# Optimization experiments

Hardware: AMD Instinct MI355X
Metric: run time of the kernel (lower is better)

## Reference

```python
import jax, jax.numpy as jnp
import numpy as np

EPS = 1e-5

def setup_inputs() -> dict:
    key = jax.random.key(0)
    ks = jax.random.split(key, 12)
    B, S = 48, 1024
    x = jax.random.normal(ks[0], (3, B, S, 3), dtype=jnp.float32)
    # stacked per-band projection weights: index 0=a, 1=b, 2=c
    WQ = jax.random.normal(ks[1], (3, 3, 3), dtype=jnp.float32) * 0.3
    bQ = jax.random.normal(ks[2], (3, 3), dtype=jnp.float32) * 0.1
    WK = jax.random.normal(ks[3], (3, 3, 3), dtype=jnp.float32) * 0.3
    bK = jax.random.normal(ks[4], (3, 3), dtype=jnp.float32) * 0.1
    WV = jax.random.normal(ks[5], (3, 3, 3), dtype=jnp.float32) * 0.3
    bV = jax.random.normal(ks[6], (3, 3), dtype=jnp.float32) * 0.1
    bn_gamma = jnp.ones((9,), dtype=jnp.float32)
    bn_beta = jnp.zeros((9,), dtype=jnp.float32)
    fc_w = jax.random.normal(ks[7], (3, 9), dtype=jnp.float32) * 0.3
    fc_b = jax.random.normal(ks[8], (3,), dtype=jnp.float32) * 0.1
    return dict(x=x, WQ=WQ, bQ=bQ, WK=WK, bK=bK, WV=WV, bV=bV,
                bn_gamma=bn_gamma, bn_beta=bn_beta, fc_w=fc_w, fc_b=fc_b)

def _attn(Q, K, V):
    # Q,K,V: (B, S, 3)
    scores = jnp.einsum('bsd,btd->bst', Q, K) / jnp.sqrt(jnp.float32(3.0))
    w = jax.nn.softmax(scores, axis=-1)
    return jnp.einsum('bst,btd->bsd', w, V)

def reference(x, WQ, bQ, WK, bK, WV, bV, bn_gamma, bn_beta, fc_w, fc_b):
    # x: (3, B, S, 3) -> per-band xs[n]: (B, S, 3)
    xs = x  # band axis already leading
    # per-band projections: Q[n] = xs[n] @ WQ[n].T + bQ[n]
    Q = jnp.einsum('nbsd,ned->nbse', xs, WQ) + bQ[:, None, None, :]
    K = jnp.einsum('nbsd,ned->nbse', xs, WK) + bK[:, None, None, :]
    V = jnp.einsum('nbsd,ned->nbse', xs, WV) + bV[:, None, None, :]
    a1 = _attn(Q[2], K[0], V[1])  # Q_c, K_a, V_b
    a2 = _attn(Q[0], K[1], V[2])  # Q_a, K_b, V_c
    a3 = _attn(Q[1], K[2], V[0])  # Q_b, K_c, V_a
    out = jnp.concatenate([a1, a2, a3], axis=-1)  # (B, S, 9)
    flat = out.reshape(-1, 9)
    # BatchNorm1d (training-mode batch statistics, biased variance)
    mean = jnp.mean(flat, axis=0)
    var = jnp.var(flat, axis=0)
    normed = (flat - mean) / jnp.sqrt(var + EPS) * bn_gamma + bn_beta
    y = normed @ fc_w.T + fc_b  # (B*S, 3)
    return y.reshape(-1, 3, 3)
```

## Files before the change

kernel.cpp:

```cpp
#include <hip/hip_runtime.h>
#include <math.h>

#define BB 48
#define SS 1024
#define NCB (3 * BB)
#define NROW (BB * SS)
#define NBLK2 (NROW / 256)

typedef float f32x2 __attribute__((ext_vector_type(2)));


template <int KSv>
__global__ __launch_bounds__(256) void mbfca_attn(
    const float* __restrict__ x,
    const float* __restrict__ WQ, const float* __restrict__ bQ,
    const float* __restrict__ WK, const float* __restrict__ bK,
    const float* __restrict__ WV, const float* __restrict__ bV,
    float* __restrict__ part)
{
    constexpr int SSK = SS / KSv;
    const int bid   = blockIdx.x;
    const int slice = bid % KSv;
    const int cb    = bid / KSv;
    const int c     = cb / BB;
    const int b     = cb % BB;
    const int kband = c;
    const int vband = (c + 1) % 3;
    const int qband = (c + 2) % 3;

    __shared__ __align__(16) float Ksm[3][SSK];
    __shared__ __align__(16) float Vsm[3][SSK];

    const int tid = threadIdx.x;

    float wk[9], wv[9], wq[9], bk[3], bv[3], bq[3];
    #pragma unroll
    for (int i = 0; i < 9; ++i) {
        wk[i] = WK[kband * 9 + i];
        wv[i] = WV[vband * 9 + i];
        wq[i] = WQ[qband * 9 + i];
    }
    #pragma unroll
    for (int i = 0; i < 3; ++i) {
        bk[i] = bK[kband * 3 + i];
        bv[i] = bV[vband * 3 + i];
        bq[i] = bQ[qband * 3 + i];
    }

    const float* xk = x + (size_t)(kband * BB + b) * SS * 3;
    const float* xv = x + (size_t)(vband * BB + b) * SS * 3;
    const float* xq = x + (size_t)(qband * BB + b) * SS * 3;

    for (int t = tid; t < SSK; t += 256) {
        const int tk = slice * SSK + t;
        float a0 = xk[tk * 3 + 0], a1 = xk[tk * 3 + 1], a2 = xk[tk * 3 + 2];
        Ksm[0][t] = wk[0] * a0 + wk[1] * a1 + wk[2] * a2 + bk[0];
        Ksm[1][t] = wk[3] * a0 + wk[4] * a1 + wk[5] * a2 + bk[1];
        Ksm[2][t] = wk[6] * a0 + wk[7] * a1 + wk[8] * a2 + bk[2];
        float c0 = xv[tk * 3 + 0], c1 = xv[tk * 3 + 1], c2 = xv[tk * 3 + 2];
        Vsm[0][t] = wv[0] * c0 + wv[1] * c1 + wv[2] * c2 + bv[0];
        Vsm[1][t] = wv[3] * c0 + wv[4] * c1 + wv[5] * c2 + bv[1];
        Vsm[2][t] = wv[6] * c0 + wv[7] * c1 + wv[8] * c2 + bv[2];
    }
    __syncthreads();

    const float qscale = 0.57735026918962576f * 1.4426950408889634f;
    f32x2 qp0[4], qp1[4], qp2[4];
    {
        const float4* xq4 = reinterpret_cast<const float4*>(xq + 12 * tid);
        float4 A = xq4[0], B4 = xq4[1], C4 = xq4[2];
        float a[12] = {A.x, A.y, A.z, A.w, B4.x, B4.y, B4.z, B4.w,
                       C4.x, C4.y, C4.z, C4.w};
        #pragma unroll
        for (int j = 0; j < 4; ++j) {
            float a0 = a[j * 3 + 0], a1 = a[j * 3 + 1], a2 = a[j * 3 + 2];
            float t0 = (wq[0] * a0 + wq[1] * a1 + wq[2] * a2 + bq[0]) * qscale;
            float t1 = (wq[3] * a0 + wq[4] * a1 + wq[5] * a2 + bq[1]) * qscale;
            float t2 = (wq[6] * a0 + wq[7] * a1 + wq[8] * a2 + bq[2]) * qscale;
            qp0[j] = (f32x2){t0, t0};
            qp1[j] = (f32x2){t1, t1};
            qp2[j] = (f32x2){t2, t2};
        }
    }

    f32x2 lac[4], a0[4], a1[4], a2[4];
    #pragma unroll
    for (int j = 0; j < 4; ++j) {
        lac[j] = (f32x2){0.f, 0.f};
        a0[j]  = (f32x2){0.f, 0.f};
        a1[j]  = (f32x2){0.f, 0.f};
        a2[j]  = (f32x2){0.f, 0.f};
    }

    const float4* K0 = reinterpret_cast<const float4*>(&Ksm[0][0]);
    const float4* K1 = reinterpret_cast<const float4*>(&Ksm[1][0]);
    const float4* K2 = reinterpret_cast<const float4*>(&Ksm[2][0]);
    const float4* V0 = reinterpret_cast<const float4*>(&Vsm[0][0]);
    const float4* V1 = reinterpret_cast<const float4*>(&Vsm[1][0]);
    const float4* V2 = reinterpret_cast<const float4*>(&Vsm[2][0]);

    for (int t4 = 0; t4 < SSK / 4; ++t4) {
        float4 k0 = K0[t4], k1 = K1[t4], k2 = K2[t4];
        float4 v0 = V0[t4], v1 = V1[t4], v2 = V2[t4];
        f32x2 k0l = {k0.x, k0.y}, k0h = {k0.z, k0.w};
        f32x2 k1l = {k1.x, k1.y}, k1h = {k1.z, k1.w};
        f32x2 k2l = {k2.x, k2.y}, k2h = {k2.z, k2.w};
        f32x2 v0l = {v0.x, v0.y}, v0h = {v0.z, v0.w};
        f32x2 v1l = {v1.x, v1.y}, v1h = {v1.z, v1.w};
        f32x2 v2l = {v2.x, v2.y}, v2h = {v2.z, v2.w};
        #pragma unroll
        for (int j = 0; j < 4; ++j) {
            f32x2 sl = qp0[j] * k0l + qp1[j] * k1l + qp2[j] * k2l;
            f32x2 sh = qp0[j] * k0h + qp1[j] * k1h + qp2[j] * k2h;
            f32x2 pl, ph;
            pl.x = __builtin_amdgcn_exp2f(sl.x);
            pl.y = __builtin_amdgcn_exp2f(sl.y);
            ph.x = __builtin_amdgcn_exp2f(sh.x);
            ph.y = __builtin_amdgcn_exp2f(sh.y);
            lac[j] += pl + ph;
            a0[j]  += pl * v0l + ph * v0h;
            a1[j]  += pl * v1l + ph * v1h;
            a2[j]  += pl * v2l + ph * v2h;
        }
    }

    float4* dst = reinterpret_cast<float4*>(part) +
                  ((size_t)(slice * NCB + cb) * SS + 4 * tid);
    #pragma unroll
    for (int j = 0; j < 4; ++j)
        dst[j] = make_float4(a0[j].x + a0[j].y,
                             a1[j].x + a1[j].y,
                             a2[j].x + a2[j].y,
                             lac[j].x + lac[j].y);
}

template <int KSv>
__global__ __launch_bounds__(256) void mbfca_stats(
    float* __restrict__ part, float* __restrict__ partial)
{
    const int r = blockIdx.x * 256 + threadIdx.x;
    const int b = r >> 10, s = r & 1023;
    __shared__ float red[4][18];

    float sums[18];
    #pragma unroll
    for (int k = 0; k < 18; ++k) sums[k] = 0.f;

    float4* p4 = reinterpret_cast<float4*>(part);
    #pragma unroll
    for (int c = 0; c < 3; ++c) {
        const int cb = c * BB + b;
        float4 t = make_float4(0.f, 0.f, 0.f, 0.f);
        #pragma unroll
        for (int sl = 0; sl < KSv; ++sl) {
            float4 u = p4[(size_t)(sl * NCB + cb) * SS + s];
            t.x += u.x; t.y += u.y; t.z += u.z; t.w += u.w;
        }
        float inv = 1.0f / t.w;
        float o0 = t.x * inv, o1 = t.y * inv, o2 = t.z * inv;
        p4[(size_t)cb * SS + s] = make_float4(o0, o1, o2, 0.f);
        sums[3 * c + 0] = o0;          sums[3 * c + 1] = o1;          sums[3 * c + 2] = o2;
        sums[9 + 3 * c + 0] = o0 * o0; sums[9 + 3 * c + 1] = o1 * o1; sums[9 + 3 * c + 2] = o2 * o2;
    }

    #pragma unroll
    for (int off = 32; off >= 1; off >>= 1)
        #pragma unroll
        for (int k = 0; k < 18; ++k)
            sums[k] += __shfl_xor(sums[k], off, 64);

    const int tid = threadIdx.x;
    if ((tid & 63) == 0) {
        #pragma unroll
        for (int k = 0; k < 18; ++k) red[tid >> 6][k] = sums[k];
    }
    __syncthreads();
    if (tid < 18)
        partial[blockIdx.x * 18 + tid] =
            red[0][tid] + red[1][tid] + red[2][tid] + red[3][tid];
}

__global__ __launch_bounds__(256) void mbfca_bnfc(
    const float* __restrict__ part, const float* __restrict__ partial,
    const float* __restrict__ gamma, const float* __restrict__ beta,
    const float* __restrict__ fcw, const float* __restrict__ fcb,
    float* __restrict__ out)
{
    __shared__ float red[4][18];
    __shared__ float accs[18];
    const int tid = threadIdx.x;

    float sums[18];
    #pragma unroll
    for (int k = 0; k < 18; ++k) sums[k] = 0.f;
    if (tid < NBLK2) {
        #pragma unroll
        for (int k = 0; k < 18; ++k) sums[k] = partial[tid * 18 + k];
    }
    #pragma unroll
    for (int off = 32; off >= 1; off >>= 1)
        #pragma unroll
        for (int k = 0; k < 18; ++k)
            sums[k] += __shfl_xor(sums[k], off, 64);
    if ((tid & 63) == 0) {
        #pragma unroll
        for (int k = 0; k < 18; ++k) red[tid >> 6][k] = sums[k];
    }
    __syncthreads();
    if (tid < 18)
        accs[tid] = red[0][tid] + red[1][tid] + red[2][tid] + red[3][tid];
    __syncthreads();

    const int r = blockIdx.x * 256 + tid;
    const int b = r >> 10, s = r & 1023;
    const float invN = 1.0f / (float)NROW;

    float sc[9], sh[9];
    #pragma unroll
    for (int ch = 0; ch < 9; ++ch) {
        float mean = accs[ch] * invN;
        float var  = accs[9 + ch] * invN - mean * mean;
        float sfac = gamma[ch] * rsqrtf(var + 1e-5f);
        sc[ch] = sfac;
        sh[ch] = beta[ch] - mean * sfac;
    }

    const float4* p4 = reinterpret_cast<const float4*>(part);
    float y0 = fcb[0], y1 = fcb[1], y2 = fcb[2];
    #pragma unroll
    for (int c = 0; c < 3; ++c) {
        const int cb = c * BB + b;
        float4 t = p4[(size_t)cb * SS + s];
        float o[3] = {t.x, t.y, t.z};
        #pragma unroll
        for (int e = 0; e < 3; ++e) {
            float n = o[e] * sc[3 * c + e] + sh[3 * c + e];
            y0 += n * fcw[3 * c + e];
            y1 += n * fcw[9 + 3 * c + e];
            y2 += n * fcw[18 + 3 * c + e];
        }
    }
    out[r * 3 + 0] = y0;
    out[r * 3 + 1] = y1;
    out[r * 3 + 2] = y2;
}

extern "C" void kernel_launch(void* const* d_in, const int* in_sizes, int n_in,
                              void* d_out, int out_size, void* d_ws, size_t ws_size,
                              hipStream_t stream)
{
    const float* x     = (const float*)d_in[0];
    const float* WQ    = (const float*)d_in[1];
    const float* bQv   = (const float*)d_in[2];
    const float* WK    = (const float*)d_in[3];
    const float* bKv   = (const float*)d_in[4];
    const float* WV    = (const float*)d_in[5];
    const float* bVv   = (const float*)d_in[6];
    const float* gamma = (const float*)d_in[7];
    const float* beta  = (const float*)d_in[8];
    const float* fcw   = (const float*)d_in[9];
    const float* fcb   = (const float*)d_in[10];

    float* part = (float*)d_ws;

    const size_t need8 = (size_t)8 * NCB * SS * 4 * sizeof(float)
                       + (size_t)NBLK2 * 18 * sizeof(float);

    if (ws_size >= need8) {
        float* partial = part + (size_t)8 * NCB * SS * 4;
        mbfca_attn<8><<<dim3(NCB * 8), dim3(256), 0, stream>>>(
            x, WQ, bQv, WK, bKv, WV, bVv, part);
        mbfca_stats<8><<<dim3(NBLK2), dim3(256), 0, stream>>>(part, partial);
        mbfca_bnfc<<<dim3(NBLK2), dim3(256), 0, stream>>>(
            part, partial, gamma, beta, fcw, fcb, (float*)d_out);
    } else {
        float* partial = part + (size_t)4 * NCB * SS * 4;
        mbfca_attn<4><<<dim3(NCB * 4), dim3(256), 0, stream>>>(
            x, WQ, bQv, WK, bKv, WV, bVv, part);
        mbfca_stats<4><<<dim3(NBLK2), dim3(256), 0, stream>>>(part, partial);
        mbfca_bnfc<<<dim3(NBLK2), dim3(256), 0, stream>>>(
            part, partial, gamma, beta, fcw, fcb, (float*)d_out);
    }
}
```

Baseline: 54.27 us.

## Precompute K/V/Q projections and stream K/V via scalar loads in attention

Adds a projection kernel that computes K and V once per (band-pair, batch) into an interleaved quad layout, and Q pre-scaled into a separate buffer. The attention kernel then reads K/V tiles through wave-uniform scalar loads (s_load_dwordx16/x8) instead of staging them in LDS. This removes redundant projection work across slices, the LDS fill, and the barrier. In exchange it adds a kernel launch, a global round trip for the projections, and an s_waitcnt on every iteration that may stall the loop. The LDS path remains as a fallback when workspace is small.

Result: slower. 62.61 us (+15.4%).

```diff
diff --git a/kernel.cpp b/kernel.cpp
--- a/kernel.cpp
+++ b/kernel.cpp
@@ -6,12 +6,188 @@
 #define NCB (3 * BB)
 #define NROW (BB * SS)
 #define NBLK2 (NROW / 256)
+#define NQUAD 256
 
 typedef float f32x2 __attribute__((ext_vector_type(2)));
-
+typedef int   i32x16 __attribute__((ext_vector_type(16)));
+typedef int   i32x8  __attribute__((ext_vector_type(8)));
+
+#define KV_FLOATS ((size_t)NCB * NQUAD * 24)
+#define QH_FLOATS ((size_t)NCB * 3 * SS)
+
+#define SLOADW(c16, c8, p)                                           \
+    asm volatile("s_load_dwordx16 %0, %2, 0x0\n\t"                   \
+                 "s_load_dwordx8  %1, %2, 0x40\n\t"                  \
+                 "s_waitcnt lgkmcnt(0)"                              \
+                 : "=&s"(c16), "=&s"(c8) : "s"(p))
+
+__global__ __launch_bounds__(256) void mbfca_proj(
+    const float* __restrict__ x,
+    const float* __restrict__ WQ, const float* __restrict__ bQ,
+    const float* __restrict__ WK, const float* __restrict__ bK,
+    const float* __restrict__ WV, const float* __restrict__ bV,
+    float* __restrict__ KV, float* __restrict__ Qh)
+{
+    const int cb = blockIdx.x;
+    const int c  = cb / BB;
+    const int b  = cb % BB;
+    const int kband = c;
+    const int vband = (c + 1) % 3;
+    const int qband = (c + 2) % 3;
+    const int t = threadIdx.x;
+
+    const float* xk = x + (size_t)(kband * BB + b) * SS * 3;
+    const float* xv = x + (size_t)(vband * BB + b) * SS * 3;
+    const float* xq = x + (size_t)(qband * BB + b) * SS * 3;
+
+    float wk[9], wv[9], wq[9], bk[3], bv[3], bq[3];
+    const float qscale = 0.57735026918962576f * 1.4426950408889634f;
+    #pragma unroll
+    for (int i = 0; i < 9; ++i) {
+        wk[i] = WK[kband * 9 + i];
+        wv[i] = WV[vband * 9 + i];
+        wq[i] = WQ[qband * 9 + i] * qscale;
+    }
+    #pragma unroll
+    for (int i = 0; i < 3; ++i) {
+        bk[i] = bK[kband * 3 + i];
+        bv[i] = bV[vband * 3 + i];
+        bq[i] = bQ[qband * 3 + i] * qscale;
+    }
+
+    {
+        const float4* k4 = reinterpret_cast<const float4*>(xk + 12 * t);
+        const float4* v4 = reinterpret_cast<const float4*>(xv + 12 * t);
+        float4 KA = k4[0], KB = k4[1], KC = k4[2];
+        float4 VA = v4[0], VB = v4[1], VC = v4[2];
+        float ka[12] = {KA.x, KA.y, KA.z, KA.w, KB.x, KB.y, KB.z, KB.w,
+                        KC.x, KC.y, KC.z, KC.w};
+        float va[12] = {VA.x, VA.y, VA.z, VA.w, VB.x, VB.y, VB.z, VB.w,
+                        VC.x, VC.y, VC.z, VC.w};
+        float out[24];
+        #pragma unroll
+        for (int j = 0; j < 4; ++j) {
+            float a0 = ka[3 * j], a1 = ka[3 * j + 1], a2 = ka[3 * j + 2];
+            out[0 + j]  = wk[0] * a0 + wk[1] * a1 + wk[2] * a2 + bk[0];
+            out[4 + j]  = wk[3] * a0 + wk[4] * a1 + wk[5] * a2 + bk[1];
+            out[8 + j]  = wk[6] * a0 + wk[7] * a1 + wk[8] * a2 + bk[2];
+            float c0 = va[3 * j], c1 = va[3 * j + 1], c2 = va[3 * j + 2];
+            out[12 + j] = wv[0] * c0 + wv[1] * c1 + wv[2] * c2 + bv[0];
+            out[16 + j] = wv[3] * c0 + wv[4] * c1 + wv[5] * c2 + bv[1];
+            out[20 + j] = wv[6] * c0 + wv[7] * c1 + wv[8] * c2 + bv[2];
+        }
+        float* dst = KV + ((size_t)cb * NQUAD + t) * 24;
+        #pragma unroll
+        for (int v = 0; v < 6; ++v)
+            reinterpret_cast<float4*>(dst)[v] =
+                make_float4(out[4 * v], out[4 * v + 1],
+                            out[4 * v + 2], out[4 * v + 3]);
+    }
+
+    {
+        const float4* q4 = reinterpret_cast<const float4*>(xq + 12 * t);
+        float4 QA = q4[0], QB = q4[1], QC = q4[2];
+        float qa[12] = {QA.x, QA.y, QA.z, QA.w, QB.x, QB.y, QB.z, QB.w,
+                        QC.x, QC.y, QC.z, QC.w};
+        float o[3][4];
+        #pragma unroll
+        for (int j = 0; j < 4; ++j) {
+            float a0 = qa[3 * j], a1 = qa[3 * j + 1], a2 = qa[3 * j + 2];
+            o[0][j] = wq[0] * a0 + wq[1] * a1 + wq[2] * a2 + bq[0];
+            o[1][j] = wq[3] * a0 + wq[4] * a1 + wq[5] * a2 + bq[1];
+            o[2][j] = wq[6] * a0 + wq[7] * a1 + wq[8] * a2 + bq[2];
+        }
+        float* qdst = Qh + (size_t)cb * 3 * SS;
+        #pragma unroll
+        for (int p = 0; p < 3; ++p)
+            reinterpret_cast<float4*>(qdst + (size_t)p * SS)[t] =
+                make_float4(o[p][0], o[p][1], o[p][2], o[p][3]);
+    }
+}
 
 template <int KSv>
-__global__ __launch_bounds__(256) void mbfca_attn(
+__global__ __launch_bounds__(256) void mbfca_attn_s(
+    const float* __restrict__ KV, const float* __restrict__ Qh,
+    float* __restrict__ part)
+{
+    constexpr int NIT = (SS / KSv) / 4;
+    const int bid   = blockIdx.x;
+    const int slice = bid % KSv;
+    const int cb    = bid / KSv;
+    const int tid   = threadIdx.x;
+
+    const float* qb = Qh + (size_t)cb * 3 * SS;
+    float4 qv0 = reinterpret_cast<const float4*>(qb + 0 * SS)[tid];
+    float4 qv1 = reinterpret_cast<const float4*>(qb + 1 * SS)[tid];
+    float4 qv2 = reinterpret_cast<const float4*>(qb + 2 * SS)[tid];
+    f32x2 qp0[4] = {{qv0.x,qv0.x},{qv0.y,qv0.y},{qv0.z,qv0.z},{qv0.w,qv0.w}};
+    f32x2 qp1[4] = {{qv1.x,qv1.x},{qv1.y,qv1.y},{qv1.z,qv1.z},{qv1.w,qv1.w}};
+    f32x2 qp2[4] = {{qv2.x,qv2.x},{qv2.y,qv2.y},{qv2.z,qv2.z},{qv2.w,qv2.w}};
+
+    f32x2 lac[4], a0[4], a1[4], a2[4];
+    #pragma unroll
+    for (int j = 0; j < 4; ++j) {
+        lac[j] = (f32x2){0.f, 0.f};
+        a0[j]  = (f32x2){0.f, 0.f};
+        a1[j]  = (f32x2){0.f, 0.f};
+        a2[j]  = (f32x2){0.f, 0.f};
+    }
+
+    const float* kv = KV + ((size_t)cb * NQUAD + slice * NIT) * 24;
+
+    for (int t = 0; t < NIT; ++t) {
+        i32x16 c16;
+        i32x8  c8;
+        SLOADW(c16, c8, kv + (size_t)t * 24);
+
+        f32x2 k0l = {__int_as_float(c16[0]),  __int_as_float(c16[1])};
+        f32x2 k0h = {__int_as_float(c16[2]),  __int_as_float(c16[3])};
+        f32x2 k1l = {__int_as_float(c16[4]),  __int_as_float(c16[5])};
+        f32x2 k1h = {__int_as_float(c16[6]),  __int_as_float(c16[7])};
+        f32x2 k2l = {__int_as_float(c16[8]),  __int_as_float(c16[9])};
+        f32x2 k2h = {__int_as_float(c16[10]), __int_as_float(c16[11])};
+        f32x2 v0l = {__int_as_float(c16[12]), __int_as_float(c16[13])};
+        f32x2 v0h = {__int_as_float(c16[14]), __int_as_float(c16[15])};
+        f32x2 v1l = {__int_as_float(c8[0]),   __int_as_float(c8[1])};
+        f32x2 v1h = {__int_as_float(c8[2]),   __int_as_float(c8[3])};
+        f32x2 v2l = {__int_as_float(c8[4]),   __int_as_float(c8[5])};
+        f32x2 v2h = {__int_as_float(c8[6]),   __int_as_float(c8[7])};
+
+        f32x2 sl[4], sh[4];
+        #pragma unroll
+        for (int j = 0; j < 4; ++j) {
+            sl[j] = qp0[j] * k0l + qp1[j] * k1l + qp2[j] * k2l;
+            sh[j] = qp0[j] * k0h + qp1[j] * k1h + qp2[j] * k2h;
+        }
+        f32x2 pl[4], ph[4];
+        #pragma unroll
+        for (int j = 0; j < 4; ++j) {
+            pl[j].x = __builtin_amdgcn_exp2f(sl[j].x);
+            pl[j].y = __builtin_amdgcn_exp2f(sl[j].y);
+            ph[j].x = __builtin_amdgcn_exp2f(sh[j].x);
+            ph[j].y = __builtin_amdgcn_exp2f(sh[j].y);
+        }
+        #pragma unroll
+        for (int j = 0; j < 4; ++j) {
+            lac[j] += pl[j] + ph[j];
+            a0[j]  += pl[j] * v0l + ph[j] * v0h;
+            a1[j]  += pl[j] * v1l + ph[j] * v1h;
+            a2[j]  += pl[j] * v2l + ph[j] * v2h;
+        }
+    }
+
+    float4* dst = reinterpret_cast<float4*>(part) +
+                  ((size_t)(slice * NCB + cb) * SS + 4 * tid);
+    #pragma unroll
+    for (int j = 0; j < 4; ++j)
+        dst[j] = make_float4(a0[j].x + a0[j].y,
+                             a1[j].x + a1[j].y,
+                             a2[j].x + a2[j].y,
+                             lac[j].x + lac[j].y);
+}
+
+template <int KSv>
+__global__ __launch_bounds__(256) void mbfca_attn_lds(
     const float* __restrict__ x,
     const float* __restrict__ WQ, const float* __restrict__ bQ,
     const float* __restrict__ WK, const float* __restrict__ bK,
@@ -24,59 +200,54 @@
     const int cb    = bid / KSv;
     const int c     = cb / BB;
     const int b     = cb % BB;
-    const int kband = c;
-    const int vband = (c + 1) % 3;
-    const int qband = (c + 2) % 3;
+    const int kband = c, vband = (c + 1) % 3, qband = (c + 2) % 3;
 
     __shared__ __align__(16) float Ksm[3][SSK];
     __shared__ __align__(16) float Vsm[3][SSK];
-
     const int tid = threadIdx.x;
-
-    float wk[9], wv[9], wq[9], bk[3], bv[3], bq[3];
-    #pragma unroll
-    for (int i = 0; i < 9; ++i) {
-        wk[i] = WK[kband * 9 + i];
-        wv[i] = WV[vband * 9 + i];
-        wq[i] = WQ[qband * 9 + i];
-    }
-    #pragma unroll
-    for (int i = 0; i < 3; ++i) {
-        bk[i] = bK[kband * 3 + i];
-        bv[i] = bV[vband * 3 + i];
-        bq[i] = bQ[qband * 3 + i];
-    }
 
     const float* xk = x + (size_t)(kband * BB + b) * SS * 3;
     const float* xv = x + (size_t)(vband * BB + b) * SS * 3;
     const float* xq = x + (size_t)(qband * BB + b) * SS * 3;
 
-    for (int t = tid; t < SSK; t += 256) {
-        const int tk = slice * SSK + t;
-        float a0 = xk[tk * 3 + 0], a1 = xk[tk * 3 + 1], a2 = xk[tk * 3 + 2];
-        Ksm[0][t] = wk[0] * a0 + wk[1] * a1 + wk[2] * a2 + bk[0];
-        Ksm[1][t] = wk[3] * a0 + wk[4] * a1 + wk[5] * a2 + bk[1];
-        Ksm[2][t] = wk[6] * a0 + wk[7] * a1 + wk[8] * a2 + bk[2];
-        float c0 = xv[tk * 3 + 0], c1 = xv[tk * 3 + 1], c2 = xv[tk * 3 + 2];
-        Vsm[0][t] = wv[0] * c0 + wv[1] * c1 + wv[2] * c2 + bv[0];
-        Vsm[1][t] = wv[3] * c0 + wv[4] * c1 + wv[5] * c2 + bv[1];
-        Vsm[2][t] = wv[6] * c0 + wv[7] * c1 + wv[8] * c2 + bv[2];
+    {
+        float wk[9], wv[9], bk[3], bv[3];
+        #pragma unroll
+        for (int i = 0; i < 9; ++i) { wk[i] = WK[kband * 9 + i]; wv[i] = WV[vband * 9 + i]; }
+        #pragma unroll
+        for (int i = 0; i < 3; ++i) { bk[i] = bK[kband * 3 + i]; bv[i] = bV[vband * 3 + i]; }
+        for (int t = tid; t < SSK; t += 256) {
+            const int tk = slice * SSK + t;
+            float a0 = xk[tk * 3 + 0], a1 = xk[tk * 3 + 1], a2 = xk[tk * 3 + 2];
+            Ksm[0][t] = wk[0] * a0 + wk[1] * a1 + wk[2] * a2 + bk[0];
+            Ksm[1][t] = wk[3] * a0 + wk[4] * a1 + wk[5] * a2 + bk[1];
+            Ksm[2][t] = wk[6] * a0 + wk[7] * a1 + wk[8] * a2 + bk[2];
+            float c0 = xv[tk * 3 + 0], c1 = xv[tk * 3 + 1], c2 = xv[tk * 3 + 2];
+            Vsm[0][t] = wv[0] * c0 + wv[1] * c1 + wv[2] * c2 + bv[0];
+            Vsm[1][t] = wv[3] * c0 + wv[4] * c1 + wv[5] * c2 + bv[1];
+            Vsm[2][t] = wv[6] * c0 + wv[7] * c1 + wv[8] * c2 + bv[2];
+        }
     }
     __syncthreads();
 
-    const float qscale = 0.57735026918962576f * 1.4426950408889634f;
     f32x2 qp0[4], qp1[4], qp2[4];
     {
+        float wq[9], bq[3];
+        const float qscale = 0.57735026918962576f * 1.4426950408889634f;
+        #pragma unroll
+        for (int i = 0; i < 9; ++i) wq[i] = WQ[qband * 9 + i] * qscale;
+        #pragma unroll
+        for (int i = 0; i < 3; ++i) bq[i] = bQ[qband * 3 + i] * qscale;
         const float4* xq4 = reinterpret_cast<const float4*>(xq + 12 * tid);
         float4 A = xq4[0], B4 = xq4[1], C4 = xq4[2];
         float a[12] = {A.x, A.y, A.z, A.w, B4.x, B4.y, B4.z, B4.w,
                        C4.x, C4.y, C4.z, C4.w};
         #pragma unroll
         for (int j = 0; j < 4; ++j) {
-            float a0 = a[j * 3 + 0], a1 = a[j * 3 + 1], a2 = a[j * 3 + 2];
-            float t0 = (wq[0] * a0 + wq[1] * a1 + wq[2] * a2 + bq[0]) * qscale;
-            float t1 = (wq[3] * a0 + wq[4] * a1 + wq[5] * a2 + bq[1]) * qscale;
-            float t2 = (wq[6] * a0 + wq[7] * a1 + wq[8] * a2 + bq[2]) * qscale;
+            float a0 = a[3 * j], a1 = a[3 * j + 1], a2 = a[3 * j + 2];
+            float t0 = wq[0] * a0 + wq[1] * a1 + wq[2] * a2 + bq[0];
+            float t1 = wq[3] * a0 + wq[4] * a1 + wq[5] * a2 + bq[1];
+            float t2 = wq[6] * a0 + wq[7] * a1 + wq[8] * a2 + bq[2];
             qp0[j] = (f32x2){t0, t0};
             qp1[j] = (f32x2){t1, t1};
             qp2[j] = (f32x2){t2, t2};
@@ -261,21 +432,29 @@
     const float* fcw   = (const float*)d_in[9];
     const float* fcb   = (const float*)d_in[10];
 
-    float* part = (float*)d_ws;
-
-    const size_t need8 = (size_t)8 * NCB * SS * 4 * sizeof(float)
-                       + (size_t)NBLK2 * 18 * sizeof(float);
-
-    if (ws_size >= need8) {
-        float* partial = part + (size_t)8 * NCB * SS * 4;
-        mbfca_attn<8><<<dim3(NCB * 8), dim3(256), 0, stream>>>(
-            x, WQ, bQv, WK, bKv, WV, bVv, part);
-        mbfca_stats<8><<<dim3(NBLK2), dim3(256), 0, stream>>>(part, partial);
+    float* ws = (float*)d_ws;
+
+    constexpr int KS = 8;
+    const size_t part_f = (size_t)KS * NCB * SS * 4;
+    const size_t need_s = (part_f + KV_FLOATS + QH_FLOATS
+                           + (size_t)NBLK2 * 18) * sizeof(float);
+
+    if (ws_size >= need_s) {
+        float* part    = ws;
+        float* KV      = part + part_f;
+        float* Qh      = KV + KV_FLOATS;
+        float* partial = Qh + QH_FLOATS;
+        mbfca_proj<<<dim3(NCB), dim3(256), 0, stream>>>(
+            x, WQ, bQv, WK, bKv, WV, bVv, KV, Qh);
+        mbfca_attn_s<KS><<<dim3(NCB * KS), dim3(256), 0, stream>>>(
+            KV, Qh, part);
+        mbfca_stats<KS><<<dim3(NBLK2), dim3(256), 0, stream>>>(part, partial);
         mbfca_bnfc<<<dim3(NBLK2), dim3(256), 0, stream>>>(
             part, partial, gamma, beta, fcw, fcb, (float*)d_out);
     } else {
+        float* part    = ws;
         float* partial = part + (size_t)4 * NCB * SS * 4;
-        mbfca_attn<4><<<dim3(NCB * 4), dim3(256), 0, stream>>>(
+        mbfca_attn_lds<4><<<dim3(NCB * 4), dim3(256), 0, stream>>>(
             x, WQ, bQv, WK, bKv, WV, bVv, part);
         mbfca_stats<4><<<dim3(NBLK2), dim3(256), 0, stream>>>(part, partial);
         mbfca_bnfc<<<dim3(NBLK2), dim3(256), 0, stream>>>(
```
